# Kernel optimization log

Hardware: AMD Instinct MI355X
Metric: run time of the kernel (lower is better)

Reference implementation:

```python
import jax, jax.numpy as jnp
import numpy as np
from functools import partial

T, B, IN, H, OUT = 512, 64, 512, 1024, 512


def _qrnn_layer(x, W, b):
    """One QRNN layer (window=1, fo-pool). x: (T,B,D) -> (T,B,H)."""
    g = jnp.einsum('tbd,dh->tbh', x, W) + b        # (T,B,3H)
    z, f, o = jnp.split(g, 3, axis=-1)
    z = jnp.tanh(z)
    f = jax.nn.sigmoid(f)
    o = jax.nn.sigmoid(o)

    def step(c, zf):
        z_t, f_t = zf
        c = f_t * c + (1.0 - f_t) * z_t            # fo-pool recurrence
        return c, c

    c0 = jnp.zeros((x.shape[1], W.shape[1] // 3), x.dtype)
    _, cs = jax.lax.scan(step, c0, (z, f))         # cs: (T,B,H)
    return o * cs


def setup_inputs() -> dict:
    key = jax.random.key(0)
    ks = jax.random.split(key, 5)
    scale = lambda fan_in: 1.0 / np.sqrt(fan_in)
    return {
        'x':   jax.random.normal(ks[0], (T, B, IN), jnp.float32),
        'W0':  jax.random.normal(ks[1], (IN, 3 * H), jnp.float32) * scale(IN),
        'b0':  jnp.zeros((3 * H,), jnp.float32),
        'W1':  jax.random.normal(ks[2], (H, 3 * H), jnp.float32) * scale(H),
        'b1':  jnp.zeros((3 * H,), jnp.float32),
        'Wfc': jax.random.normal(ks[3], (H, OUT), jnp.float32) * scale(H),
        'bfc': jnp.zeros((OUT,), jnp.float32),
    }


def reference(x, W0, b0, W1, b1, Wfc, bfc):
    h = _qrnn_layer(x, W0, b0)                     # layer 0: (T,B,H)
    h = _qrnn_layer(h, W1, b1)                     # layer 1: (T,B,H)
    out = jnp.einsum('tbh,ho->tbo', h, Wfc) + bfc  # fc over all timesteps
    return out
```

## Files before the change

kernel.cpp:

```cpp
#include <hip/hip_runtime.h>
#include <hip/hip_bf16.h>


#define QT 512
#define QB 64
#define QIN 512
#define QH 1024
#define QOUT 512
#define QM (QT * QB)
#define SEG 32
#define SL (QT / SEG)

typedef unsigned short ushort_t;
typedef __attribute__((ext_vector_type(8))) short bf16x8;
typedef __attribute__((ext_vector_type(4))) float f32x4;

__device__ __forceinline__ float u2f(ushort_t u) {
    union { unsigned int i; float f; } v;
    v.i = ((unsigned int)u) << 16;
    return v.f;
}

__device__ __forceinline__ float blo(unsigned int u) {
    union { unsigned int i; float f; } v;
    v.i = u << 16;
    return v.f;
}

__device__ __forceinline__ float bhi(unsigned int u) {
    union { unsigned int i; float f; } v;
    v.i = u & 0xffff0000u;
    return v.f;
}

__device__ __forceinline__ ushort_t f2bf(float f) {
    union { float f; unsigned int i; } v;
    v.f = f;
    unsigned int r = v.i + 0x7fffu + ((v.i >> 16) & 1u);
    return (ushort_t)(r >> 16);
}

__device__ __forceinline__ void glds16(const ushort_t* g, ushort_t* l) {
    __builtin_amdgcn_global_load_lds(
        (const __attribute__((address_space(1))) void*)g,
        (__attribute__((address_space(3))) void*)l, 16, 0, 0);
}

__global__ __launch_bounds__(256) void cvt_bf16(const float* __restrict__ src,
                                                ushort_t* __restrict__ dst) {
    const int i = blockIdx.x * 256 + threadIdx.x;
    float4 v = ((const float4*)src)[i];
    ushort4 o;
    o.x = f2bf(v.x); o.y = f2bf(v.y); o.z = f2bf(v.z); o.w = f2bf(v.w);
    ((ushort4*)dst)[i] = o;
}

__global__ __launch_bounds__(256) void transpose_cvt(
    const float* __restrict__ W, ushort_t* __restrict__ WT, int K, int N) {
    __shared__ float t[32][33];
    const int tx = threadIdx.x & 31, ty = threadIdx.x >> 5;
    const int n0 = blockIdx.x * 32, k0 = blockIdx.y * 32;
#pragma unroll
    for (int i = 0; i < 4; ++i)
        t[ty + 8 * i][tx] = W[(size_t)(k0 + ty + 8 * i) * N + n0 + tx];
    __syncthreads();
#pragma unroll
    for (int i = 0; i < 4; ++i)
        WT[(size_t)(n0 + ty + 8 * i) * K + k0 + tx] = f2bf(t[tx][ty + 8 * i]);
}

template <int MODE, int K>
__global__ __launch_bounds__(512, 2) void gemm256(
    const ushort_t* __restrict__ A, const ushort_t* __restrict__ BT,
    const float* __restrict__ bias, void* __restrict__ out,
    int c0, int CW) {
    constexpr int NT = K / 32;
    __shared__ ushort_t As[4 * 8192];
    __shared__ ushort_t Bs[4 * 8192];

    const int tid = threadIdx.x;
    const int lane = tid & 63;
    const int w = tid >> 6;
    const int wr = w >> 2, wc = w & 3;

    const int gx = gridDim.x;
    const int nwg = gx * gridDim.y;
    int flat = blockIdx.y * gx + blockIdx.x;
    flat = (flat & 7) * (nwg >> 3) + (flat >> 3);
    const int by = flat / gx;
    const int bx = flat - by * gx;
    const int m0 = by * 256;

    int nW, nOut, outstride, gate = 0;
    if (MODE == 0) {
        const int per = CW >> 8;
        gate = bx / per;
        const int nloc = (bx - gate * per) * 256;
        nW = gate * QH + c0 + nloc;
        nOut = gate * CW + nloc;
        outstride = 3 * CW;
    } else {
        nW = bx * 256;
        nOut = nW;
        outstride = QOUT;
    }

    size_t aoff[2], boff[2];
    int ldso[2];
#pragma unroll
    for (int j = 0; j < 2; ++j) {
        const int c = w * 128 + j * 64 + lane;
        const int r = c >> 2;
        const int gs = (c & 3) ^ ((r >> 1) & 3);
        aoff[j] = (size_t)(m0 + r) * K + gs * 8;
        boff[j] = (size_t)(nW + r) * K + gs * 8;
        ldso[j] = w * 1024 + j * 512;
    }

    const int fl = lane & 15, fq = lane >> 4;
    const int laneoff = fl * 32 + ((fq ^ ((fl >> 1) & 3)) << 3);

    f32x4 acc[8][4];
#pragma unroll
    for (int i = 0; i < 8; ++i)
#pragma unroll
        for (int j = 0; j < 4; ++j) acc[i][j] = {0.f, 0.f, 0.f, 0.f};

#pragma unroll
    for (int t = 0; t < 3; ++t) {
        const int slot = t * 8192;
#pragma unroll
        for (int j = 0; j < 2; ++j)
            glds16(A + aoff[j] + t * 32, &As[slot + ldso[j]]);
#pragma unroll
        for (int j = 0; j < 2; ++j)
            glds16(BT + boff[j] + t * 32, &Bs[slot + ldso[j]]);
    }
    asm volatile("s_waitcnt vmcnt(8)" ::: "memory");
    __builtin_amdgcn_s_barrier();

    for (int kt = 0; kt < NT; ++kt) {
        const int slot = (kt & 3) * 8192;
        const int sa = slot + wr * 4096 + laneoff;
        const int sb = slot + wc * 2048 + laneoff;
        const bool pf = (kt + 3 < NT);
        const int pslot = ((kt + 3) & 3) * 8192;
        const size_t kb = (size_t)(kt + 3) * 32;

        bf16x8 a0[4], a1[4], bv[4];
#pragma unroll
        for (int i = 0; i < 4; ++i) a0[i] = *(const bf16x8*)&As[sa + i * 512];
#pragma unroll
        for (int j = 0; j < 4; ++j) bv[j] = *(const bf16x8*)&Bs[sb + j * 512];
        if (pf) {
#pragma unroll
            for (int j = 0; j < 2; ++j)
                glds16(A + aoff[j] + kb, &As[pslot + ldso[j]]);
        }
        __builtin_amdgcn_sched_barrier(0);
        __builtin_amdgcn_s_barrier();
        asm volatile("s_waitcnt lgkmcnt(0)" ::: "memory");
        __builtin_amdgcn_sched_barrier(0);
        __builtin_amdgcn_s_setprio(1);
#pragma unroll
        for (int i = 0; i < 4; ++i)
#pragma unroll
            for (int j = 0; j < 4; ++j)
                acc[i][j] = __builtin_amdgcn_mfma_f32_16x16x32_bf16(
                    a0[i], bv[j], acc[i][j], 0, 0, 0);
        __builtin_amdgcn_s_setprio(0);
        __builtin_amdgcn_sched_barrier(0);
        __builtin_amdgcn_s_barrier();
#pragma unroll
        for (int i = 0; i < 4; ++i)
            a1[i] = *(const bf16x8*)&As[sa + (4 + i) * 512];
        if (pf) {
#pragma unroll
            for (int j = 0; j < 2; ++j)
                glds16(BT + boff[j] + kb, &Bs[pslot + ldso[j]]);
        }
        __builtin_amdgcn_sched_barrier(0);
        __builtin_amdgcn_s_barrier();
        asm volatile("s_waitcnt lgkmcnt(0)" ::: "memory");
        __builtin_amdgcn_sched_barrier(0);
        __builtin_amdgcn_s_setprio(1);
#pragma unroll
        for (int i = 0; i < 4; ++i)
#pragma unroll
            for (int j = 0; j < 4; ++j)
                acc[4 + i][j] = __builtin_amdgcn_mfma_f32_16x16x32_bf16(
                    a1[i], bv[j], acc[4 + i][j], 0, 0, 0);
        __builtin_amdgcn_s_setprio(0);
        if (kt < NT - 3)
            asm volatile("s_waitcnt vmcnt(8)" ::: "memory");
        else if (kt == NT - 3)
            asm volatile("s_waitcnt vmcnt(4)" ::: "memory");
        else if (kt == NT - 2)
            asm volatile("s_waitcnt vmcnt(0)" ::: "memory");
        __builtin_amdgcn_sched_barrier(0);
        if (kt < NT - 1) __builtin_amdgcn_s_barrier();
    }

    const float ak = (gate == 0) ? 2.8853900817779268f : -1.4426950408889634f;
    const float aa = (gate == 0) ? -2.f : 1.f;
    const float ad = (gate == 0) ? 1.f : 0.f;

    float bvv[4];
#pragma unroll
    for (int j = 0; j < 4; ++j) bvv[j] = bias[nW + wc * 64 + j * 16 + fl];
#pragma unroll
    for (int i = 0; i < 8; ++i) {
#pragma unroll
        for (int r = 0; r < 4; ++r) {
            const int row = m0 + wr * 128 + i * 16 + fq * 4 + r;
#pragma unroll
            for (int j = 0; j < 4; ++j) {
                const int col = nOut + wc * 64 + j * 16 + fl;
                float v = acc[i][j][r] + bvv[j];
                if (MODE == 0) {
                    v = aa * __builtin_amdgcn_rcpf(
                                 1.f + __builtin_amdgcn_exp2f(ak * v)) +
                        ad;
                    ((ushort_t*)out)[(size_t)row * outstride + col] = f2bf(v);
                } else {
                    ((float*)out)[(size_t)row * outstride + col] = v;
                }
            }
        }
    }
}


__global__ __launch_bounds__(256) void scan_p1(const ushort_t* __restrict__ g,
                                               float* __restrict__ Aseg,
                                               float* __restrict__ Bseg,
                                               int CW) {
    const int idx4 = blockIdx.x * 256 + threadIdx.x;
    const int cw4 = CW >> 2;
    const int hh = (idx4 % cw4) << 2;
    const int sb = idx4 / cw4;
    const int b = sb % QB;
    const int s = sb / QB;
    const ushort_t* gp = g + ((size_t)(s * SL * QB + b) * 3) * CW + hh;
    const size_t grow = (size_t)QB * 3 * CW;
    uint2 zu[SL], fu[SL];
#pragma unroll
    for (int t = 0; t < SL; ++t) {
        zu[t] = *(const uint2*)gp;
        fu[t] = *(const uint2*)(gp + CW);
        gp += grow;
    }
    float4 A = {1.f, 1.f, 1.f, 1.f}, Bc = {0.f, 0.f, 0.f, 0.f};
#pragma unroll
    for (int t = 0; t < SL; ++t) {
        const float f0 = blo(fu[t].x), f1 = bhi(fu[t].x);
        const float f2 = blo(fu[t].y), f3 = bhi(fu[t].y);
        Bc.x = f0 * Bc.x + (1.f - f0) * blo(zu[t].x);
        Bc.y = f1 * Bc.y + (1.f - f1) * bhi(zu[t].x);
        Bc.z = f2 * Bc.z + (1.f - f2) * blo(zu[t].y);
        Bc.w = f3 * Bc.w + (1.f - f3) * bhi(zu[t].y);
        A.x *= f0; A.y *= f1; A.z *= f2; A.w *= f3;
    }
    const size_t oidx = (size_t)sb * CW + hh;
    *(float4*)&Aseg[oidx] = A;
    *(float4*)&Bseg[oidx] = Bc;
}

__global__ __launch_bounds__(256) void scan_p3(const ushort_t* __restrict__ g,
                                               const float* __restrict__ Aseg,
                                               const float* __restrict__ Bseg,
                                               ushort_t* __restrict__ h,
                                               int c0, int CW) {
    const int idx4 = blockIdx.x * 256 + threadIdx.x;
    const int cw4 = CW >> 2;
    const int hh = (idx4 % cw4) << 2;
    const int sb = idx4 / cw4;
    const int b = sb % QB;
    const int s = sb / QB;
    const ushort_t* gp = g + ((size_t)(s * SL * QB + b) * 3) * CW + hh;
    ushort_t* hp = h + (size_t)(s * SL * QB + b) * QH + c0 + hh;
    const size_t grow = (size_t)QB * 3 * CW;
    const size_t hrow = (size_t)QB * QH;
    uint2 zu[SL], fu[SL], ou[SL];
#pragma unroll
    for (int t = 0; t < SL; ++t) {
        zu[t] = *(const uint2*)gp;
        fu[t] = *(const uint2*)(gp + CW);
        ou[t] = *(const uint2*)(gp + 2 * CW);
        gp += grow;
    }
    float4 c = {0.f, 0.f, 0.f, 0.f};
    const size_t stride = (size_t)QB * CW;
    const size_t colo = (size_t)b * CW + hh;
    for (int sp = 0; sp < s; ++sp) {
        const float4 Av = *(const float4*)&Aseg[sp * stride + colo];
        const float4 Bv = *(const float4*)&Bseg[sp * stride + colo];
        c.x = Av.x * c.x + Bv.x;
        c.y = Av.y * c.y + Bv.y;
        c.z = Av.z * c.z + Bv.z;
        c.w = Av.w * c.w + Bv.w;
    }
#pragma unroll
    for (int t = 0; t < SL; ++t) {
        const float f0 = blo(fu[t].x), f1 = bhi(fu[t].x);
        const float f2 = blo(fu[t].y), f3 = bhi(fu[t].y);
        c.x = f0 * c.x + (1.f - f0) * blo(zu[t].x);
        c.y = f1 * c.y + (1.f - f1) * bhi(zu[t].x);
        c.z = f2 * c.z + (1.f - f2) * blo(zu[t].y);
        c.w = f3 * c.w + (1.f - f3) * bhi(zu[t].y);
        ushort4 hv;
        hv.x = f2bf(blo(ou[t].x) * c.x);
        hv.y = f2bf(bhi(ou[t].x) * c.y);
        hv.z = f2bf(blo(ou[t].y) * c.z);
        hv.w = f2bf(bhi(ou[t].y) * c.w);
        *(ushort4*)hp = hv;
        hp += hrow;
    }
}

extern "C" void kernel_launch(void* const* d_in, const int* in_sizes, int n_in,
                              void* d_out, int out_size, void* d_ws,
                              size_t ws_size, hipStream_t stream) {
    const float* x   = (const float*)d_in[0];
    const float* W0  = (const float*)d_in[1];
    const float* b0  = (const float*)d_in[2];
    const float* W1  = (const float*)d_in[3];
    const float* b1  = (const float*)d_in[4];
    const float* Wfc = (const float*)d_in[5];
    const float* bfc = (const float*)d_in[6];
    float* out = (float*)d_out;

    char* p = (char*)d_ws;
    ushort_t* h0   = (ushort_t*)p;  p += (size_t)QM * QH * 2;
    ushort_t* h1   = (ushort_t*)p;
    ushort_t* x_bf = (ushort_t*)p;  p += (size_t)QM * QH * 2;
    ushort_t* W0T  = (ushort_t*)p;  p += (size_t)3 * QH * QIN * 2;
    ushort_t* W1T  = (ushort_t*)p;  p += (size_t)3 * QH * QH * 2;
    ushort_t* WfcT = (ushort_t*)p;  p += (size_t)QOUT * QH * 2;
    const size_t base = (size_t)(p - (char*)d_ws);

    int CW = QH;
    while (CW > 256 &&
           base + 3 * (size_t)QB * CW * SEG * 4 + (size_t)QM * 3 * CW * 2 >
               ws_size)
        CW >>= 1;
    const int nch = QH / CW;

    float* Aseg   = (float*)p;  p += (size_t)QB * CW * SEG * 4;
    float* Bseg   = (float*)p;  p += (size_t)QB * CW * SEG * 4;
    p += (size_t)QB * CW * SEG * 4;
    ushort_t* g   = (ushort_t*)p;

    dim3 blk(256);
    dim3 blk5(512);

    cvt_bf16<<<dim3(QM * QIN / 1024), blk, 0, stream>>>(x, x_bf);
    transpose_cvt<<<dim3(3 * QH / 32, QIN / 32), blk, 0, stream>>>(
        W0, W0T, QIN, 3 * QH);
    transpose_cvt<<<dim3(3 * QH / 32, QH / 32), blk, 0, stream>>>(
        W1, W1T, QH, 3 * QH);
    transpose_cvt<<<dim3(QOUT / 32, QH / 32), blk, 0, stream>>>(
        Wfc, WfcT, QH, QOUT);

    const dim3 ggrid(3 * (CW >> 8), QM / 256);
    const dim3 p13grid(SEG * QB * CW / 1024);

    for (int ci = 0; ci < nch; ++ci) {
        gemm256<0, QIN><<<ggrid, blk5, 0, stream>>>(x_bf, W0T, b0, g,
                                                    ci * CW, CW);
        scan_p1<<<p13grid, blk, 0, stream>>>(g, Aseg, Bseg, CW);
        scan_p3<<<p13grid, blk, 0, stream>>>(g, Aseg, Bseg, h0, ci * CW, CW);
    }
    for (int ci = 0; ci < nch; ++ci) {
        gemm256<0, QH><<<ggrid, blk5, 0, stream>>>(h0, W1T, b1, g,
                                                   ci * CW, CW);
        scan_p1<<<p13grid, blk, 0, stream>>>(g, Aseg, Bseg, CW);
        scan_p3<<<p13grid, blk, 0, stream>>>(g, Aseg, Bseg, h1, ci * CW, CW);
    }
    gemm256<1, QH><<<dim3(QOUT / 256, QM / 256), blk5, 0, stream>>>(
        h1, WfcT, bfc, out, 0, 0);
}
```

Baseline: 669.6 us.

## Reshape GEMM tile to 128x512 with three-stage LDS pipeline

Changes the GEMM block tile from 256x256 to 128 rows by 512 columns, so each wave computes 64x128 and reuses A fragments across two B halves instead of reusing B across two A halves. The LDS ring drops from four stages to three and is resized to fit the new A/B footprint, with prefetch distance and vmcnt waits adjusted. The minimum chunk width rises to 512 and grids are recomputed. The goal is to cut redundant A traffic and fit the tile to wide N, but this risks fewer in-flight prefetches and a fragile waitcnt schedule.

```diff
diff --git a/kernel.cpp b/kernel.cpp
--- a/kernel.cpp
+++ b/kernel.cpp
@@ -15,12 +15,6 @@
 typedef __attribute__((ext_vector_type(8))) short bf16x8;
 typedef __attribute__((ext_vector_type(4))) float f32x4;
 
-__device__ __forceinline__ float u2f(ushort_t u) {
-    union { unsigned int i; float f; } v;
-    v.i = ((unsigned int)u) << 16;
-    return v.f;
-}
-
 __device__ __forceinline__ float blo(unsigned int u) {
     union { unsigned int i; float f; } v;
     v.i = u << 16;
@@ -75,8 +69,8 @@
     const float* __restrict__ bias, void* __restrict__ out,
     int c0, int CW) {
     constexpr int NT = K / 32;
-    __shared__ ushort_t As[4 * 8192];
-    __shared__ ushort_t Bs[4 * 8192];
+    __shared__ ushort_t As[3 * 4096];
+    __shared__ ushort_t Bs[3 * 16384];
 
     const int tid = threadIdx.x;
     const int lane = tid & 63;
@@ -89,73 +83,70 @@
     flat = (flat & 7) * (nwg >> 3) + (flat >> 3);
     const int by = flat / gx;
     const int bx = flat - by * gx;
-    const int m0 = by * 256;
+    const int m0 = by * 128;
 
     int nW, nOut, outstride, gate = 0;
     if (MODE == 0) {
-        const int per = CW >> 8;
+        const int per = CW >> 9;
         gate = bx / per;
-        const int nloc = (bx - gate * per) * 256;
+        const int nloc = (bx - gate * per) * 512;
         nW = gate * QH + c0 + nloc;
         nOut = gate * CW + nloc;
         outstride = 3 * CW;
     } else {
-        nW = bx * 256;
+        nW = bx * 512;
         nOut = nW;
         outstride = QOUT;
     }
 
-    size_t aoff[2], boff[2];
-    int ldso[2];
-#pragma unroll
-    for (int j = 0; j < 2; ++j) {
-        const int c = w * 128 + j * 64 + lane;
+    const int ca = w * 64 + lane;
+    const int ra = ca >> 2;
+    size_t aoffA = (size_t)(m0 + ra) * K + ((ca & 3) ^ ((ra >> 1) & 3)) * 8;
+    const int ldsoA = w * 512;
+    size_t boffB[4];
+    int ldsoB[4];
+#pragma unroll
+    for (int t = 0; t < 4; ++t) {
+        const int c = t * 512 + w * 64 + lane;
         const int r = c >> 2;
-        const int gs = (c & 3) ^ ((r >> 1) & 3);
-        aoff[j] = (size_t)(m0 + r) * K + gs * 8;
-        boff[j] = (size_t)(nW + r) * K + gs * 8;
-        ldso[j] = w * 1024 + j * 512;
+        boffB[t] = (size_t)(nW + r) * K + ((c & 3) ^ ((r >> 1) & 3)) * 8;
+        ldsoB[t] = t * 4096 + w * 512;
     }
 
     const int fl = lane & 15, fq = lane >> 4;
     const int laneoff = fl * 32 + ((fq ^ ((fl >> 1) & 3)) << 3);
 
-    f32x4 acc[8][4];
-#pragma unroll
-    for (int i = 0; i < 8; ++i)
-#pragma unroll
-        for (int j = 0; j < 4; ++j) acc[i][j] = {0.f, 0.f, 0.f, 0.f};
-
-#pragma unroll
-    for (int t = 0; t < 3; ++t) {
-        const int slot = t * 8192;
-#pragma unroll
-        for (int j = 0; j < 2; ++j)
-            glds16(A + aoff[j] + t * 32, &As[slot + ldso[j]]);
-#pragma unroll
-        for (int j = 0; j < 2; ++j)
-            glds16(BT + boff[j] + t * 32, &Bs[slot + ldso[j]]);
-    }
-    asm volatile("s_waitcnt vmcnt(8)" ::: "memory");
+    f32x4 acc[4][8];
+#pragma unroll
+    for (int i = 0; i < 4; ++i)
+#pragma unroll
+        for (int j = 0; j < 8; ++j) acc[i][j] = {0.f, 0.f, 0.f, 0.f};
+
+#pragma unroll
+    for (int t = 0; t < 2; ++t) {
+        glds16(A + aoffA + t * 32, &As[t * 4096 + ldsoA]);
+#pragma unroll
+        for (int tt = 0; tt < 4; ++tt)
+            glds16(BT + boffB[tt] + t * 32, &Bs[t * 16384 + ldsoB[tt]]);
+    }
+    asm volatile("s_waitcnt vmcnt(5)" ::: "memory");
     __builtin_amdgcn_s_barrier();
 
+    int cur = 0, stg = 2;
     for (int kt = 0; kt < NT; ++kt) {
-        const int slot = (kt & 3) * 8192;
-        const int sa = slot + wr * 4096 + laneoff;
-        const int sb = slot + wc * 2048 + laneoff;
-        const bool pf = (kt + 3 < NT);
-        const int pslot = ((kt + 3) & 3) * 8192;
-        const size_t kb = (size_t)(kt + 3) * 32;
-
-        bf16x8 a0[4], a1[4], bv[4];
-#pragma unroll
-        for (int i = 0; i < 4; ++i) a0[i] = *(const bf16x8*)&As[sa + i * 512];
-#pragma unroll
-        for (int j = 0; j < 4; ++j) bv[j] = *(const bf16x8*)&Bs[sb + j * 512];
+        const int sA = cur * 4096 + wr * 2048 + laneoff;
+        const int sB = cur * 16384 + wc * 4096 + laneoff;
+        const bool pf = (kt + 2 < NT);
+        const size_t kb = (size_t)(kt + 2) * 32;
+
+        bf16x8 af[4], bv[4], bw[4];
+#pragma unroll
+        for (int i = 0; i < 4; ++i) af[i] = *(const bf16x8*)&As[sA + i * 512];
+#pragma unroll
+        for (int j = 0; j < 4; ++j) bv[j] = *(const bf16x8*)&Bs[sB + j * 512];
         if (pf) {
-#pragma unroll
-            for (int j = 0; j < 2; ++j)
-                glds16(A + aoff[j] + kb, &As[pslot + ldso[j]]);
+            glds16(A + aoffA + kb, &As[stg * 4096 + ldsoA]);
+            glds16(BT + boffB[0] + kb, &Bs[stg * 16384 + ldsoB[0]]);
         }
         __builtin_amdgcn_sched_barrier(0);
         __builtin_amdgcn_s_barrier();
@@ -167,17 +158,17 @@
 #pragma unroll
             for (int j = 0; j < 4; ++j)
                 acc[i][j] = __builtin_amdgcn_mfma_f32_16x16x32_bf16(
-                    a0[i], bv[j], acc[i][j], 0, 0, 0);
+                    af[i], bv[j], acc[i][j], 0, 0, 0);
         __builtin_amdgcn_s_setprio(0);
         __builtin_amdgcn_sched_barrier(0);
         __builtin_amdgcn_s_barrier();
 #pragma unroll
-        for (int i = 0; i < 4; ++i)
-            a1[i] = *(const bf16x8*)&As[sa + (4 + i) * 512];
+        for (int j = 0; j < 4; ++j)
+            bw[j] = *(const bf16x8*)&Bs[sB + (4 + j) * 512];
         if (pf) {
 #pragma unroll
-            for (int j = 0; j < 2; ++j)
-                glds16(BT + boff[j] + kb, &Bs[pslot + ldso[j]]);
+            for (int tt = 1; tt < 4; ++tt)
+                glds16(BT + boffB[tt] + kb, &Bs[stg * 16384 + ldsoB[tt]]);
         }
         __builtin_amdgcn_sched_barrier(0);
         __builtin_amdgcn_s_barrier();
@@ -188,34 +179,34 @@
         for (int i = 0; i < 4; ++i)
 #pragma unroll
             for (int j = 0; j < 4; ++j)
-                acc[4 + i][j] = __builtin_amdgcn_mfma_f32_16x16x32_bf16(
-                    a1[i], bv[j], acc[4 + i][j], 0, 0, 0);
+                acc[i][4 + j] = __builtin_amdgcn_mfma_f32_16x16x32_bf16(
+                    af[i], bw[j], acc[i][4 + j], 0, 0, 0);
         __builtin_amdgcn_s_setprio(0);
-        if (kt < NT - 3)
-            asm volatile("s_waitcnt vmcnt(8)" ::: "memory");
-        else if (kt == NT - 3)
-            asm volatile("s_waitcnt vmcnt(4)" ::: "memory");
+        if (kt < NT - 2)
+            asm volatile("s_waitcnt vmcnt(5)" ::: "memory");
         else if (kt == NT - 2)
             asm volatile("s_waitcnt vmcnt(0)" ::: "memory");
         __builtin_amdgcn_sched_barrier(0);
         if (kt < NT - 1) __builtin_amdgcn_s_barrier();
+        cur = (cur == 2) ? 0 : cur + 1;
+        stg = (stg == 2) ? 0 : stg + 1;
     }
 
     const float ak = (gate == 0) ? 2.8853900817779268f : -1.4426950408889634f;
     const float aa = (gate == 0) ? -2.f : 1.f;
     const float ad = (gate == 0) ? 1.f : 0.f;
 
-    float bvv[4];
-#pragma unroll
-    for (int j = 0; j < 4; ++j) bvv[j] = bias[nW + wc * 64 + j * 16 + fl];
-#pragma unroll
-    for (int i = 0; i < 8; ++i) {
+    float bvv[8];
+#pragma unroll
+    for (int j = 0; j < 8; ++j) bvv[j] = bias[nW + wc * 128 + j * 16 + fl];
+#pragma unroll
+    for (int i = 0; i < 4; ++i) {
 #pragma unroll
         for (int r = 0; r < 4; ++r) {
-            const int row = m0 + wr * 128 + i * 16 + fq * 4 + r;
-#pragma unroll
-            for (int j = 0; j < 4; ++j) {
-                const int col = nOut + wc * 64 + j * 16 + fl;
+            const int row = m0 + wr * 64 + i * 16 + fq * 4 + r;
+#pragma unroll
+            for (int j = 0; j < 8; ++j) {
+                const int col = nOut + wc * 128 + j * 16 + fl;
                 float v = acc[i][j][r] + bvv[j];
                 if (MODE == 0) {
                     v = aa * __builtin_amdgcn_rcpf(
@@ -340,7 +331,7 @@
     const size_t base = (size_t)(p - (char*)d_ws);
 
     int CW = QH;
-    while (CW > 256 &&
+    while (CW > 512 &&
            base + 3 * (size_t)QB * CW * SEG * 4 + (size_t)QM * 3 * CW * 2 >
                ws_size)
         CW >>= 1;
@@ -362,7 +353,7 @@
     transpose_cvt<<<dim3(QOUT / 32, QH / 32), blk, 0, stream>>>(
         Wfc, WfcT, QH, QOUT);
 
-    const dim3 ggrid(3 * (CW >> 8), QM / 256);
+    const dim3 ggrid(3 * (CW >> 9), QM / 128);
     const dim3 p13grid(SEG * QB * CW / 1024);
 
     for (int ci = 0; ci < nch; ++ci) {
@@ -377,6 +368,6 @@
         scan_p1<<<p13grid, blk, 0, stream>>>(g, Aseg, Bseg, CW);
         scan_p3<<<p13grid, blk, 0, stream>>>(g, Aseg, Bseg, h1, ci * CW, CW);
     }
-    gemm256<1, QH><<<dim3(QOUT / 256, QM / 256), blk5, 0, stream>>>(
+    gemm256<1, QH><<<dim3(QOUT / 512, QM / 128), blk5, 0, stream>>>(
         h1, WfcT, bfc, out, 0, 0);
 }
```

Measured after the change: 703.2 us. 5.0% more time.

## Software-pipeline LDS fragment loads across k-steps with double-buffered B registers

Applied to the files above, without the earlier changes.

Restructures the GEMM main loop so each k-step's A0/B fragments for the next tile are loaded from LDS during the current step, using ping-pong B register sets and a 2x manual unroll. Waits change from lgkmcnt(0) to partial counts so MFMAs can start while later LDS reads are still in flight. This aims to hide LDS read latency behind MFMA work, at the cost of more live VGPRs and subtler wait-count and barrier correctness. The vmcnt thresholds are also adjusted to the new ordering of global-to-LDS loads.

```diff
diff --git a/kernel.cpp b/kernel.cpp
--- a/kernel.cpp
+++ b/kernel.cpp
@@ -15,12 +15,6 @@
 typedef __attribute__((ext_vector_type(8))) short bf16x8;
 typedef __attribute__((ext_vector_type(4))) float f32x4;
 
-__device__ __forceinline__ float u2f(ushort_t u) {
-    union { unsigned int i; float f; } v;
-    v.i = ((unsigned int)u) << 16;
-    return v.f;
-}
-
 __device__ __forceinline__ float blo(unsigned int u) {
     union { unsigned int i; float f; } v;
     v.i = u << 16;
@@ -68,6 +62,72 @@
     for (int i = 0; i < 4; ++i)
         WT[(size_t)(n0 + ty + 8 * i) * K + k0 + tx] = f2bf(t[tx][ty + 8 * i]);
 }
+
+
+#define QSTEP(KT, BC, BN)                                                     \
+  {                                                                           \
+    const int kt = (KT);                                                      \
+    const int slot = (kt & 3) * 8192;                                         \
+    const int sa = slot + wr * 4096 + laneoff;                                \
+    const bool pf = (kt + 3 < NT);                                            \
+    const int pslot = ((kt + 3) & 3) * 8192;                                  \
+    const size_t kb = (size_t)(kt + 3) * 32;                                  \
+     \
+    _Pragma("unroll") for (int i = 0; i < 4; ++i)                             \
+        A1[i] = *(const bf16x8*)&As[sa + (4 + i) * 512];                      \
+    if (pf) {                                                                 \
+      glds16(A + aoff[0] + kb, &As[pslot + ldso[0]]);                         \
+      glds16(A + aoff[1] + kb, &As[pslot + ldso[1]]);                         \
+    }                                                                         \
+    __builtin_amdgcn_sched_barrier(0);                                        \
+    __builtin_amdgcn_s_barrier();                                             \
+    asm volatile("s_waitcnt lgkmcnt(4)" ::: "memory");                        \
+    __builtin_amdgcn_sched_barrier(0);                                        \
+    __builtin_amdgcn_s_setprio(1);                                            \
+    _Pragma("unroll") for (int i = 0; i < 4; ++i)                             \
+        _Pragma("unroll") for (int j = 0; j < 4; ++j)                         \
+            acc[i][j] = __builtin_amdgcn_mfma_f32_16x16x32_bf16(              \
+                A0[i], BC[j], acc[i][j], 0, 0, 0);                            \
+    __builtin_amdgcn_s_setprio(0);                                            \
+    __builtin_amdgcn_sched_barrier(0);                                        \
+    if (kt < NT - 3)                                                          \
+      asm volatile("s_waitcnt vmcnt(6)" ::: "memory");                        \
+    else if (kt == NT - 3)                                                    \
+      asm volatile("s_waitcnt vmcnt(4)" ::: "memory");                        \
+    else if (kt == NT - 2)                                                    \
+      asm volatile("s_waitcnt vmcnt(0)" ::: "memory");                        \
+    __builtin_amdgcn_sched_barrier(0);                                        \
+    __builtin_amdgcn_s_barrier();     \
+     \
+    if (kt < NT - 1) {                                                        \
+      const int sn = ((kt + 1) & 3) * 8192;                                   \
+      const int sa2 = sn + wr * 4096 + laneoff;                               \
+      const int sb2 = sn + wc * 2048 + laneoff;                               \
+      _Pragma("unroll") for (int j = 0; j < 4; ++j)                           \
+          BN[j] = *(const bf16x8*)&Bs[sb2 + j * 512];                         \
+      _Pragma("unroll") for (int i = 0; i < 4; ++i)                           \
+          A0[i] = *(const bf16x8*)&As[sa2 + i * 512];                         \
+    }                                                                         \
+    if (pf) {                                                                 \
+      glds16(BT + boff[0] + kb, &Bs[pslot + ldso[0]]);                        \
+      glds16(BT + boff[1] + kb, &Bs[pslot + ldso[1]]);                        \
+    }                                                                         \
+    __builtin_amdgcn_sched_barrier(0);                                        \
+    __builtin_amdgcn_s_barrier();                                             \
+    if (kt < NT - 1)                                                          \
+      asm volatile("s_waitcnt lgkmcnt(8)" ::: "memory");                      \
+    else                                                                      \
+      asm volatile("s_waitcnt lgkmcnt(0)" ::: "memory");                      \
+    __builtin_amdgcn_sched_barrier(0);                                        \
+    __builtin_amdgcn_s_setprio(1);                                            \
+    _Pragma("unroll") for (int i = 0; i < 4; ++i)                             \
+        _Pragma("unroll") for (int j = 0; j < 4; ++j)                         \
+            acc[4 + i][j] = __builtin_amdgcn_mfma_f32_16x16x32_bf16(          \
+                A1[i], BC[j], acc[4 + i][j], 0, 0, 0);                        \
+    __builtin_amdgcn_s_setprio(0);                                            \
+    __builtin_amdgcn_sched_barrier(0);                                        \
+    if (kt < NT - 1) __builtin_amdgcn_s_barrier();                            \
+  }
 
 template <int MODE, int K>
 __global__ __launch_bounds__(512, 2) void gemm256(
@@ -129,76 +189,28 @@
 #pragma unroll
     for (int t = 0; t < 3; ++t) {
         const int slot = t * 8192;
-#pragma unroll
-        for (int j = 0; j < 2; ++j)
-            glds16(A + aoff[j] + t * 32, &As[slot + ldso[j]]);
-#pragma unroll
-        for (int j = 0; j < 2; ++j)
-            glds16(BT + boff[j] + t * 32, &Bs[slot + ldso[j]]);
+        glds16(A + aoff[0] + t * 32, &As[slot + ldso[0]]);
+        glds16(A + aoff[1] + t * 32, &As[slot + ldso[1]]);
+        glds16(BT + boff[0] + t * 32, &Bs[slot + ldso[0]]);
+        glds16(BT + boff[1] + t * 32, &Bs[slot + ldso[1]]);
     }
     asm volatile("s_waitcnt vmcnt(8)" ::: "memory");
     __builtin_amdgcn_s_barrier();
 
-    for (int kt = 0; kt < NT; ++kt) {
-        const int slot = (kt & 3) * 8192;
-        const int sa = slot + wr * 4096 + laneoff;
-        const int sb = slot + wc * 2048 + laneoff;
-        const bool pf = (kt + 3 < NT);
-        const int pslot = ((kt + 3) & 3) * 8192;
-        const size_t kb = (size_t)(kt + 3) * 32;
-
-        bf16x8 a0[4], a1[4], bv[4];
-#pragma unroll
-        for (int i = 0; i < 4; ++i) a0[i] = *(const bf16x8*)&As[sa + i * 512];
-#pragma unroll
-        for (int j = 0; j < 4; ++j) bv[j] = *(const bf16x8*)&Bs[sb + j * 512];
-        if (pf) {
-#pragma unroll
-            for (int j = 0; j < 2; ++j)
-                glds16(A + aoff[j] + kb, &As[pslot + ldso[j]]);
-        }
-        __builtin_amdgcn_sched_barrier(0);
-        __builtin_amdgcn_s_barrier();
-        asm volatile("s_waitcnt lgkmcnt(0)" ::: "memory");
-        __builtin_amdgcn_sched_barrier(0);
-        __builtin_amdgcn_s_setprio(1);
-#pragma unroll
-        for (int i = 0; i < 4; ++i)
-#pragma unroll
-            for (int j = 0; j < 4; ++j)
-                acc[i][j] = __builtin_amdgcn_mfma_f32_16x16x32_bf16(
-                    a0[i], bv[j], acc[i][j], 0, 0, 0);
-        __builtin_amdgcn_s_setprio(0);
-        __builtin_amdgcn_sched_barrier(0);
-        __builtin_amdgcn_s_barrier();
-#pragma unroll
-        for (int i = 0; i < 4; ++i)
-            a1[i] = *(const bf16x8*)&As[sa + (4 + i) * 512];
-        if (pf) {
-#pragma unroll
-            for (int j = 0; j < 2; ++j)
-                glds16(BT + boff[j] + kb, &Bs[pslot + ldso[j]]);
-        }
-        __builtin_amdgcn_sched_barrier(0);
-        __builtin_amdgcn_s_barrier();
-        asm volatile("s_waitcnt lgkmcnt(0)" ::: "memory");
-        __builtin_amdgcn_sched_barrier(0);
-        __builtin_amdgcn_s_setprio(1);
-#pragma unroll
-        for (int i = 0; i < 4; ++i)
-#pragma unroll
-            for (int j = 0; j < 4; ++j)
-                acc[4 + i][j] = __builtin_amdgcn_mfma_f32_16x16x32_bf16(
-                    a1[i], bv[j], acc[4 + i][j], 0, 0, 0);
-        __builtin_amdgcn_s_setprio(0);
-        if (kt < NT - 3)
-            asm volatile("s_waitcnt vmcnt(8)" ::: "memory");
-        else if (kt == NT - 3)
-            asm volatile("s_waitcnt vmcnt(4)" ::: "memory");
-        else if (kt == NT - 2)
-            asm volatile("s_waitcnt vmcnt(0)" ::: "memory");
-        __builtin_amdgcn_sched_barrier(0);
-        if (kt < NT - 1) __builtin_amdgcn_s_barrier();
+    bf16x8 A0[4], A1[4], Bx[4], By[4];
+    {
+        const int sa0 = wr * 4096 + laneoff;
+        const int sb0 = wc * 2048 + laneoff;
+#pragma unroll
+        for (int i = 0; i < 4; ++i) A0[i] = *(const bf16x8*)&As[sa0 + i * 512];
+#pragma unroll
+        for (int j = 0; j < 4; ++j) Bx[j] = *(const bf16x8*)&Bs[sb0 + j * 512];
+    }
+
+#pragma unroll 1
+    for (int k2 = 0; k2 < NT / 2; ++k2) {
+        QSTEP(2 * k2, Bx, By)
+        QSTEP(2 * k2 + 1, By, Bx)
     }
 
     const float ak = (gate == 0) ? 2.8853900817779268f : -1.4426950408889634f;
```

Measured after the change: 672.1 us. Within noise of the previous version (+0.4%).
